# Optimization experiments

Hardware: AMD Instinct MI355X
Metric: run time of the kernel (lower is better)

The kernel has to match this reference:

```python
import jax, jax.numpy as jnp
import numpy as np
from jax import lax

N_QUBITS = 8
N_BLOCKS = 5

_H = jnp.array([[1.0, 1.0], [1.0, -1.0]], dtype=jnp.complex64) / np.sqrt(2.0).astype(np.float32)
# torchquantum PauliY.diagonalizing_gates = [Z, S, H] applied in order -> matrix H @ S @ Z = H @ diag(1, -1j)
_YROT = _H @ jnp.diag(jnp.array([1.0, -1j], dtype=jnp.complex64))


def apply_gate(st, U, wires):
    # st: [N, 2, 2, ..., 2] (n_qubits trailing axes); U: [2^k, 2^k]
    k = len(wires)
    axes = [w + 1 for w in wires]
    s = jnp.moveaxis(st, axes, list(range(1, k + 1)))
    shp = s.shape
    s = s.reshape(shp[0], 2 ** k, -1)
    s = jnp.einsum('ij,bjr->bir', U, s)
    return jnp.moveaxis(s.reshape(shp), list(range(1, k + 1)), axes)


def u3_mat(th, ph, lam):
    c = jnp.cos(0.5 * th).astype(jnp.complex64)
    s = jnp.sin(0.5 * th).astype(jnp.complex64)
    el = jnp.exp(1j * lam)
    ep = jnp.exp(1j * ph)
    return jnp.stack([jnp.stack([c, -el * s]), jnp.stack([ep * s, ep * el * c])])


def cu3_mat(th, ph, lam):
    M = jnp.eye(4, dtype=jnp.complex64)
    return M.at[2:, 2:].set(u3_mat(th, ph, lam))


def z_expvals(st):
    # <Z_w> for every wire from marginal probabilities
    n = st.ndim - 1
    mag = st.real ** 2 + st.imag ** 2
    outs = []
    for w in range(n):
        axes = tuple(a for a in range(1, n + 1) if a != w + 1)
        p = mag.sum(axes)  # [N, 2]
        outs.append(p[:, 0] - p[:, 1])
    return jnp.stack(outs, axis=1)


def quantum_conv(x, conv_w, conv_b, u3_params, cu3_params, fc_w, fc_b):
    n = N_QUBITS
    B, C, H, W = x.shape
    y = lax.conv_general_dilated(x, conv_w, (1, 1), 'SAME',
                                 dimension_numbers=('NCHW', 'OIHW', 'NCHW'))
    y = y + conv_b[None, :, None, None]
    ang = y.transpose(0, 2, 3, 1).reshape(-1, n)  # [B*H*W, n_qubits]
    Npx = ang.shape[0]
    # RY(theta)|0> encoding: product state of [cos(t/2), sin(t/2)] per wire
    c = jnp.cos(0.5 * ang)
    s = jnp.sin(0.5 * ang)
    st = jnp.stack([c[:, 0], s[:, 0]], axis=1).astype(jnp.complex64)
    for w in range(1, n):
        q = jnp.stack([c[:, w], s[:, w]], axis=1).astype(jnp.complex64)
        st = (st[:, :, None] * q[:, None, :]).reshape(Npx, -1)
    st = st.reshape((Npx,) + (2,) * n)
    # U3CU3Layer0: per block, U3 on each wire then circular CU3 ring
    for b in range(N_BLOCKS):
        for w in range(n):
            st = apply_gate(st, u3_mat(u3_params[b, w, 0], u3_params[b, w, 1], u3_params[b, w, 2]), [w])
        for w in range(n):
            st = apply_gate(st, cu3_mat(cu3_params[b, w, 0], cu3_params[b, w, 1], cu3_params[b, w, 2]), [w, (w + 1) % n])
    # MeasureAll(Z), then MeasureAll(X) and MeasureAll(Y) which MUTATE the device
    # state with their diagonalizing gates (torchquantum semantics)
    mz = z_expvals(st)
    for w in range(n):
        st = apply_gate(st, _H, [w])
    mx = z_expvals(st)
    for w in range(n):
        st = apply_gate(st, _YROT, [w])
    my = z_expvals(st)
    meas = jnp.concatenate([mz, mx, my], axis=1)  # [B*H*W, 3*n]
    out = meas @ fc_w.T + fc_b
    return out.reshape(B, H, W, -1).transpose(0, 3, 1, 2)


def setup_inputs() -> dict:
    key = jax.random.key(0)
    ks = jax.random.split(key, 7)
    n, cin, cout = N_QUBITS, 16, 32
    x = jax.random.normal(ks[0], (4, cin, 64, 64), dtype=jnp.float32)
    conv_w = jax.random.normal(ks[1], (n, cin, 3, 3), dtype=jnp.float32) / np.sqrt(cin * 9)
    conv_b = jax.random.normal(ks[2], (n,), dtype=jnp.float32) * 0.01
    u3_params = jax.random.uniform(ks[3], (N_BLOCKS, n, 3), dtype=jnp.float32, minval=-np.pi, maxval=np.pi)
    cu3_params = jax.random.uniform(ks[4], (N_BLOCKS, n, 3), dtype=jnp.float32, minval=-np.pi, maxval=np.pi)
    fc_w = jax.random.normal(ks[5], (cout, 3 * n), dtype=jnp.float32) / np.sqrt(3 * n)
    fc_b = jax.random.normal(ks[6], (cout,), dtype=jnp.float32) * 0.01
    return {'x': x, 'conv_w': conv_w, 'conv_b': conv_b, 'u3_params': u3_params,
            'cu3_params': cu3_params, 'fc_w': fc_w, 'fc_b': fc_b}


def reference(x, conv_w, conv_b, u3_params, cu3_params, fc_w, fc_b):
    return quantum_conv(x, conv_w, conv_b, u3_params, cu3_params, fc_w, fc_b)
```

## Files before the change

### kernel.cpp

```cpp
#include <hip/hip_runtime.h>

typedef float v2f __attribute__((ext_vector_type(2)));

template<int C>
__device__ __forceinline__ float dppmov(float x) {
  return __int_as_float(__builtin_amdgcn_update_dpp(0, __float_as_int(x), C, 0xF, 0xF, true));
}
template<int IMM>
__device__ __forceinline__ float dswz(float x) {
  return __int_as_float(__builtin_amdgcn_ds_swizzle(__float_as_int(x), IMM));
}
__device__ __forceinline__ float bperm(float x, int a) {
  return __int_as_float(__builtin_amdgcn_ds_bpermute(a, __float_as_int(x)));
}
template<int M>
__device__ __forceinline__ float bfly(float x) {
  if constexpr (M == 1)      return dppmov<0xB1>(x);
  else if constexpr (M == 2) return dppmov<0x4E>(x);
  else if constexpr (M == 8) return dppmov<0x128>(x);
  else                       return dswz<0x101F>(x);
}
template<int M>
__device__ __forceinline__ v2f bfly2(v2f v) {
  v2f o; o.x = bfly<M>(v.x); o.y = bfly<M>(v.y); return o;
}
__device__ __forceinline__ v2f sp(float s) { v2f v; v.x = s; v.y = s; return v; }
__device__ __forceinline__ v2f vfma(v2f a, v2f b, v2f c) {
  return __builtin_elementwise_fma(a, b, c);
}

template<int M, int CM>
__device__ __forceinline__ void crossG(v2f Sr[16], v2f Si[16],
    const float* g, int lane) {
  const bool hi = (lane & M) != 0;
  float fr, fi, gr, gi;
  if constexpr (CM == 0) {
    fr = hi ? g[6] : g[0]; fi = hi ? g[7] : g[1];
    gr = hi ? g[4] : g[2]; gi = hi ? g[5] : g[3];
  } else {
    const bool ct = (lane & CM) != 0;
    float f0r = hi ? g[6]  : g[0],  f0i = hi ? g[7]  : g[1];
    float g0r = hi ? g[4]  : g[2],  g0i = hi ? g[5]  : g[3];
    float f1r = hi ? g[14] : g[8],  f1i = hi ? g[15] : g[9];
    float g1r = hi ? g[12] : g[10], g1i = hi ? g[13] : g[11];
    fr = ct ? f1r : f0r; fi = ct ? f1i : f0i;
    gr = ct ? g1r : g0r; gi = ct ? g1i : g0i;
  }
  v2f vfr = sp(fr), vfi = sp(fi), vgr = sp(gr), vgi = sp(gi);
  v2f vfiN = sp(-fi), vgiN = sp(-gi);
#pragma unroll
  for (int r = 0; r < 16; ++r) {
    v2f pR = bfly2<M>(Sr[r]);
    v2f pI = bfly2<M>(Si[r]);
    v2f nR = vfma(vgiN, pI, vfma(vgr, pR, vfma(vfiN, Si[r], vfr * Sr[r])));
    v2f nI = vfma(vgi,  pR, vfma(vgr, pI, vfma(vfi,  Sr[r], vfr * Si[r])));
    Sr[r] = nR; Si[r] = nI;
  }
}

__device__ __forceinline__ void mixP(v2f& x0r, v2f& x0i, v2f& x1r, v2f& x1i,
    float m0r, float m0i, float m1r, float m1i,
    float m2r, float m2i, float m3r, float m3i) {
  v2f n0r = vfma(sp(-m1i), x1i, vfma(sp(m1r), x1r, vfma(sp(-m0i), x0i, sp(m0r) * x0r)));
  v2f n0i = vfma(sp( m1i), x1r, vfma(sp(m1r), x1i, vfma(sp( m0i), x0r, sp(m0r) * x0i)));
  v2f n1r = vfma(sp(-m3i), x1i, vfma(sp(m3r), x1r, vfma(sp(-m2i), x0i, sp(m2r) * x0r)));
  v2f n1i = vfma(sp( m3i), x1r, vfma(sp(m3r), x1i, vfma(sp( m2i), x0r, sp(m2r) * x0i)));
  x0r = n0r; x0i = n0i; x1r = n1r; x1i = n1i;
}

__device__ __forceinline__ void f4N(v2f Sr[16], v2f Si[16],
    const float* g, int lane) {
  const bool ct = (lane & 1) != 0;
  float m[8];
#pragma unroll
  for (int jj = 0; jj < 8; ++jj) m[jj] = ct ? g[8 + jj] : g[jj];
#pragma unroll
  for (int r = 0; r < 8; ++r)
    mixP(Sr[r], Si[r], Sr[r + 8], Si[r + 8],
         m[0], m[1], m[2], m[3], m[4], m[5], m[6], m[7]);
}
__device__ __forceinline__ void f5N(v2f Sr[16], v2f Si[16], const float* g) {
#pragma unroll
  for (int r = 0; r < 4; ++r)
    mixP(Sr[r], Si[r], Sr[r + 4], Si[r + 4],
         g[0], g[1], g[2], g[3], g[4], g[5], g[6], g[7]);
#pragma unroll
  for (int r = 8; r < 12; ++r)
    mixP(Sr[r], Si[r], Sr[r + 4], Si[r + 4],
         g[8], g[9], g[10], g[11], g[12], g[13], g[14], g[15]);
}
__device__ __forceinline__ void f6N(v2f Sr[16], v2f Si[16], const float* g) {
#pragma unroll
  for (int t = 0; t < 4; ++t) {
    const int r0 = (t >> 1) * 8 + (t & 1);
    mixP(Sr[r0], Si[r0], Sr[r0 + 2], Si[r0 + 2],
         g[0], g[1], g[2], g[3], g[4], g[5], g[6], g[7]);
    const int r1 = r0 + 4;
    mixP(Sr[r1], Si[r1], Sr[r1 + 2], Si[r1 + 2],
         g[8], g[9], g[10], g[11], g[12], g[13], g[14], g[15]);
  }
}
__device__ __forceinline__ void f7N(v2f Sr[16], v2f Si[16], const float* g) {
#pragma unroll
  for (int t = 0; t < 4; ++t) {
    const int r0 = t * 4;
    mixP(Sr[r0], Si[r0], Sr[r0 + 1], Si[r0 + 1],
         g[0], g[1], g[2], g[3], g[4], g[5], g[6], g[7]);
    const int r1 = r0 + 2;
    mixP(Sr[r1], Si[r1], Sr[r1 + 1], Si[r1 + 1],
         g[8], g[9], g[10], g[11], g[12], g[13], g[14], g[15]);
  }
}
__device__ __forceinline__ void f8pN(v2f Sr[16], v2f Si[16],
    const float* g, int lane) {
  const bool hi = (lane & 8) != 0;
  float fr[2], fi[2], gr[2], gi[2];
  fr[0] = hi ? g[6]  : g[0];  fi[0] = hi ? g[7]  : g[1];
  gr[0] = hi ? g[4]  : g[2];  gi[0] = hi ? g[5]  : g[3];
  fr[1] = hi ? g[14] : g[8];  fi[1] = hi ? g[15] : g[9];
  gr[1] = hi ? g[12] : g[10]; gi[1] = hi ? g[13] : g[11];
#pragma unroll
  for (int r = 0; r < 16; ++r) {
    const int m = r & 1;
    v2f pR = bfly2<8>(Sr[r]);
    v2f pI = bfly2<8>(Si[r]);
    v2f nR = vfma(sp(-gi[m]), pI, vfma(sp(gr[m]), pR, vfma(sp(-fi[m]), Si[r], sp(fr[m]) * Sr[r])));
    v2f nI = vfma(sp( gi[m]), pR, vfma(sp(gr[m]), pI, vfma(sp( fi[m]), Sr[r], sp(fr[m]) * Si[r])));
    Sr[r] = nR; Si[r] = nI;
  }
}
__device__ __forceinline__ void f8N(v2f Sr[16], v2f Si[16],
    const float* g, int lane) {
  const bool hi = (lane & 8) != 0;
  const float fr = hi ? g[6] : g[0], fi = hi ? g[7] : g[1];
  const float gr = hi ? g[4] : g[2], gi = hi ? g[5] : g[3];
#pragma unroll
  for (int r = 1; r < 16; r += 2) {
    v2f pR = bfly2<8>(Sr[r]);
    v2f pI = bfly2<8>(Si[r]);
    v2f nR = vfma(sp(-gi), pI, vfma(sp(gr), pR, vfma(sp(-fi), Si[r], sp(fr) * Sr[r])));
    v2f nI = vfma(sp( gi), pR, vfma(sp(gr), pI, vfma(sp( fi), Sr[r], sp(fr) * Si[r])));
    Sr[r] = nR; Si[r] = nI;
  }
}

template<int M>
__device__ __forceinline__ void crossO(const v2f Sr[16], const v2f Si[16],
                                       v2f& re, v2f& im) {
  v2f r = sp(0.0f), i = sp(0.0f);
#pragma unroll
  for (int k = 0; k < 16; ++k) {
    v2f pr = bfly2<M>(Sr[k]);
    v2f pi = bfly2<M>(Si[k]);
    r = vfma(Sr[k], pr, r);
    r = vfma(Si[k], pi, r);
    i = vfma(Si[k], pr, i);
    i = vfma(-Sr[k], pi, i);
  }
  re = r; im = i;
}

__device__ __forceinline__ void mm2(const float* A, const float* B, float* D) {
  D[0] = A[0]*B[0] - A[1]*B[1] + A[2]*B[4] - A[3]*B[5];
  D[1] = A[0]*B[1] + A[1]*B[0] + A[2]*B[5] + A[3]*B[4];
  D[2] = A[0]*B[2] - A[1]*B[3] + A[2]*B[6] - A[3]*B[7];
  D[3] = A[0]*B[3] + A[1]*B[2] + A[2]*B[7] + A[3]*B[6];
  D[4] = A[4]*B[0] - A[5]*B[1] + A[6]*B[4] - A[7]*B[5];
  D[5] = A[4]*B[1] + A[5]*B[0] + A[6]*B[5] + A[7]*B[4];
  D[6] = A[4]*B[2] - A[5]*B[3] + A[6]*B[6] - A[7]*B[7];
  D[7] = A[4]*B[3] + A[5]*B[2] + A[6]*B[7] + A[7]*B[6];
}
__device__ __forceinline__ void u3fill(const float* src, float* o) {
  float th = src[0], ph = src[1], lam = src[2];
  float c = cosf(0.5f * th), s = sinf(0.5f * th);
  float cl = cosf(lam), sl = sinf(lam);
  float cp = cosf(ph), spv = sinf(ph);
  float cpl = cosf(ph + lam), spl = sinf(ph + lam);
  o[0] = c;        o[1] = 0.0f;
  o[2] = -cl * s;  o[3] = -sl * s;
  o[4] = cp * s;   o[5] = spv * s;
  o[6] = cpl * c;  o[7] = spl * c;
}

__global__ __launch_bounds__(256) void qconv_kernel(
    const float* __restrict__ x, const float* __restrict__ cw,
    const float* __restrict__ cb, const float* __restrict__ u3p,
    const float* __restrict__ cu3p, const float* __restrict__ fcw,
    const float* __restrict__ fcb, float* __restrict__ out) {
  __shared__ float Us[40][8];
  __shared__ float Cs[40][8];
  __shared__ float Gs[640];
  __shared__ float FCWs[768];

  {
    const int t = threadIdx.x;
    if (t < 40) u3fill(u3p + t * 3, Us[t]);
    if (t >= 64 && t < 104) u3fill(cu3p + (t - 64) * 3, Cs[t - 64]);
    __syncthreads();
    if (t == 0) {
#pragma unroll
      for (int j = 0; j < 8; ++j) Gs[j] = Us[0][j];
    } else if (t < 36) {
      int j = t - 1, b = j / 7, k = j % 7;
      float* dst = Gs + 8 + b * 112 + k * 16;
      const float* U = Us[b * 8 + k + 1];
      const float* C = Cs[b * 8 + k];
#pragma unroll
      for (int u = 0; u < 8; ++u) dst[u] = U[u];
      mm2(C, U, dst + 8);
    } else if (t < 40) {
      int b = t - 36;
      float* dst = Gs + 568 + b * 16;
      const float* U = Us[(b + 1) * 8];
      const float* C = Cs[b * 8 + 7];
#pragma unroll
      for (int u = 0; u < 8; ++u) dst[u] = U[u];
      mm2(U, C, dst + 8);
    } else if (t == 40) {
#pragma unroll
      for (int j = 0; j < 8; ++j) Gs[632 + j] = Cs[39][j];
    }
    for (int i = t; i < 768; i += 256) {
      int tt = i % 24;
      int stage = tt >> 3, w = tt & 7;
      float sc = (stage >= 1 && w >= 4) ? 2.0f : 1.0f;
      FCWs[i] = fcw[i] * sc;
    }
    __syncthreads();
  }

  const int lane = threadIdx.x & 63;
  const int wid = __builtin_amdgcn_readfirstlane(
      (int)((blockIdx.x * blockDim.x + threadIdx.x) >> 6));
  const int p0 = wid * 8;
  const int q = lane & 15;

  float ang;
  {
    const int px = lane >> 3;
    const int oc = lane & 7;
    const int p  = p0 + px;
    const int b  = p >> 12;
    const int hh = (p >> 6) & 63;
    const int wim = p & 63;
    float acc = cb[oc];
#pragma unroll 4
    for (int ic = 0; ic < 16; ++ic) {
      const float* wp = cw + (oc * 16 + ic) * 9;
      const float* xp = x + (b * 16 + ic) * 4096;
#pragma unroll
      for (int kh = 0; kh < 3; ++kh) {
        int ih = hh + kh - 1;
        bool rok = (unsigned)ih < 64u;
        int ihc = rok ? ih : 0;
#pragma unroll
        for (int kw = 0; kw < 3; ++kw) {
          int iw = wim + kw - 1;
          bool ok = rok && ((unsigned)iw < 64u);
          int iwc = ((unsigned)iw < 64u) ? iw : 0;
          float xv = xp[ihc * 64 + iwc];
          acc = fmaf(ok ? xv : 0.0f, wp[kh * 3 + kw], acc);
        }
      }
    }
    ang = acc;
  }

  v2f Sr[16], Si[16];
  {
    const int gb = (lane & 48) << 2;
    float aA[8], aB[8];
#pragma unroll
    for (int w = 0; w < 8; ++w) {
      aA[w] = bperm(ang, gb + (w << 2));
      aB[w] = bperm(ang, gb + ((8 + w) << 2));
    }
    float cA[8], sA[8], cB[8], sB[8];
#pragma unroll
    for (int w = 0; w < 8; ++w) {
      __sincosf(0.5f * aA[w], &sA[w], &cA[w]);
      __sincosf(0.5f * aB[w], &sB[w], &cB[w]);
    }
    v2f c0; c0.x = cA[0]; c0.y = cB[0];
    v2f s0; s0.x = sA[0]; s0.y = sB[0];
    v2f c0r = vfma(sp(Gs[2]), s0, sp(Gs[0]) * c0);
    v2f c0i = vfma(sp(Gs[3]), s0, sp(Gs[1]) * c0);
    v2f s0r = vfma(sp(Gs[6]), s0, sp(Gs[4]) * c0);
    v2f s0i = vfma(sp(Gs[7]), s0, sp(Gs[5]) * c0);
    const bool w0 = (q & 8) != 0;
    v2f selR = w0 ? s0r : c0r;
    v2f selI = w0 ? s0i : c0i;
    float fA = ((q & 4) ? sA[1] : cA[1]) * ((q & 2) ? sA[2] : cA[2])
             * ((q & 1) ? sA[3] : cA[3]);
    float fB = ((q & 4) ? sB[1] : cB[1]) * ((q & 2) ? sB[2] : cB[2])
             * ((q & 1) ? sB[3] : cB[3]);
    v2f uu[4], vv[4];
    uu[0].x = cA[6]*cA[7]; uu[1].x = cA[6]*sA[7];
    uu[2].x = sA[6]*cA[7]; uu[3].x = sA[6]*sA[7];
    uu[0].y = cB[6]*cB[7]; uu[1].y = cB[6]*sB[7];
    uu[2].y = sB[6]*cB[7]; uu[3].y = sB[6]*sB[7];
    float vA0 = fA * cA[4], vA1 = fA * sA[4];
    float vB0 = fB * cB[4], vB1 = fB * sB[4];
    vv[0].x = vA0*cA[5]; vv[1].x = vA0*sA[5];
    vv[2].x = vA1*cA[5]; vv[3].x = vA1*sA[5];
    vv[0].y = vB0*cB[5]; vv[1].y = vB0*sB[5];
    vv[2].y = vB1*cB[5]; vv[3].y = vB1*sB[5];
#pragma unroll
    for (int r = 0; r < 16; ++r) {
      v2f base = vv[r >> 2] * uu[r & 3];
      Sr[r] = selR * base;
      Si[r] = selI * base;
    }
  }

  for (int b = 0; b < 5; ++b) {
    const float* base = Gs + 8 + b * 112;
    crossG<4, 8>(Sr, Si, base +  0, lane);
    crossG<2, 4>(Sr, Si, base + 16, lane);
    crossG<1, 2>(Sr, Si, base + 32, lane);
    f4N(Sr, Si, base + 48, lane);
    f5N(Sr, Si, base + 64);
    f6N(Sr, Si, base + 80);
    f7N(Sr, Si, base + 96);
    if (b < 4) f8pN(Sr, Si, Gs + 568 + b * 16, lane);
  }
  f8N(Sr, Si, Gs + 632, lane);

  float sg[4];
  sg[0] = (q & 8) ? -1.0f : 1.0f;
  sg[1] = (q & 4) ? -1.0f : 1.0f;
  sg[2] = (q & 2) ? -1.0f : 1.0f;
  sg[3] = (q & 1) ? -1.0f : 1.0f;

  v2f PT[24];
  {
    v2f re0, im0, re1, im1, re2, im2, re3, im3;
    crossO<8>(Sr, Si, re0, im0);
    crossO<4>(Sr, Si, re1, im1);
    crossO<2>(Sr, Si, re2, im2);
    crossO<1>(Sr, Si, re3, im3);
    PT[8]  = re0; PT[9]  = re1; PT[10] = re2; PT[11] = re3;
    PT[16] = sp(sg[0]) * im0; PT[17] = sp(sg[1]) * im1;
    PT[18] = sp(sg[2]) * im2; PT[19] = sp(sg[3]) * im3;

    v2f P[16];
#pragma unroll
    for (int r = 0; r < 16; ++r) P[r] = vfma(Si[r], Si[r], Sr[r] * Sr[r]);
    v2f t01[8];
#pragma unroll
    for (int k = 0; k < 8; ++k) t01[k] = P[2*k] + P[2*k+1];
    v2f q0 = t01[0] + t01[1], q1 = t01[2] + t01[3];
    v2f q2 = t01[4] + t01[5], q3 = t01[6] + t01[7];
    v2f h0 = q0 + q1, h1 = q2 + q3;
    v2f p  = h0 + h1;
    PT[4] = h0 - h1;
    PT[5] = (q0 - q1) + (q2 - q3);
    PT[6] = (t01[0]-t01[1]) + (t01[2]-t01[3])
          + (t01[4]-t01[5]) + (t01[6]-t01[7]);
    PT[7] = (P[0]-P[1]) + (P[2]-P[3]) + (P[4]-P[5]) + (P[6]-P[7])
          + (P[8]-P[9]) + (P[10]-P[11]) + (P[12]-P[13]) + (P[14]-P[15]);
    PT[0] = sp(sg[0]) * p; PT[1] = sp(sg[1]) * p;
    PT[2] = sp(sg[2]) * p; PT[3] = sp(sg[3]) * p;

    v2f re, im;
    re = sp(0.0f); im = sp(0.0f);
#pragma unroll
    for (int r = 0; r < 8; ++r) {
      re = vfma(Sr[r], Sr[r+8], re); re = vfma(Si[r], Si[r+8], re);
      im = vfma(Si[r], Sr[r+8], im); im = vfma(-Sr[r], Si[r+8], im);
    }
    PT[12] = re; PT[20] = im;
    re = sp(0.0f); im = sp(0.0f);
#pragma unroll
    for (int t = 0; t < 8; ++t) {
      const int lo = (t & 3) + (t >> 2) * 8;
      re = vfma(Sr[lo], Sr[lo+4], re); re = vfma(Si[lo], Si[lo+4], re);
      im = vfma(Si[lo], Sr[lo+4], im); im = vfma(-Sr[lo], Si[lo+4], im);
    }
    PT[13] = re; PT[21] = im;
    re = sp(0.0f); im = sp(0.0f);
#pragma unroll
    for (int t = 0; t < 8; ++t) {
      const int lo = (t & 1) + (t >> 1) * 4;
      re = vfma(Sr[lo], Sr[lo+2], re); re = vfma(Si[lo], Si[lo+2], re);
      im = vfma(Si[lo], Sr[lo+2], im); im = vfma(-Sr[lo], Si[lo+2], im);
    }
    PT[14] = re; PT[22] = im;
    re = sp(0.0f); im = sp(0.0f);
#pragma unroll
    for (int t = 0; t < 8; ++t) {
      const int lo = 2 * t;
      re = vfma(Sr[lo], Sr[lo+1], re); re = vfma(Si[lo], Si[lo+1], re);
      im = vfma(Si[lo], Sr[lo+1], im); im = vfma(-Sr[lo], Si[lo+1], im);
    }
    PT[15] = re; PT[23] = im;
  }

  const int j = q & 7;
  const bool isB = (q & 8) != 0;
  float mm[24];
#pragma unroll
  for (int t = 0; t < 24; ++t) {
    v2f v = PT[t] + bfly2<8>(PT[t]);
    float s = isB ? v.y : v.x;
    s += bfly<1>(s);
    s += bfly<2>(s);
    s += bfly<4>(s);
    mm[t] = s;
  }

  const int g = lane >> 4;
  const int p = p0 + 2 * g + (isB ? 1 : 0);
  const int ob = (p >> 12) * 131072 + (p & 4095);
#pragma unroll
  for (int k = 0; k < 4; ++k) {
    const int ch = 4 * j + k;
    const float* wr = FCWs + ch * 24;
    float acc = fcb[ch];
#pragma unroll
    for (int u = 0; u < 24; ++u) acc = fmaf(mm[u], wr[u], acc);
    out[ob + ch * 4096] = acc;
  }
}

extern "C" void kernel_launch(void* const* d_in, const int* in_sizes, int n_in,
                              void* d_out, int out_size, void* d_ws, size_t ws_size,
                              hipStream_t stream) {
  const float* x      = (const float*)d_in[0];
  const float* conv_w = (const float*)d_in[1];
  const float* conv_b = (const float*)d_in[2];
  const float* u3p    = (const float*)d_in[3];
  const float* cu3p   = (const float*)d_in[4];
  const float* fcw    = (const float*)d_in[5];
  const float* fcb    = (const float*)d_in[6];
  float* out = (float*)d_out;

  qconv_kernel<<<512, 256, 0, stream>>>(x, conv_w, conv_b, u3p, cu3p,
                                        fcw, fcb, out);
}
```

Before: 107.0 us.

## Fuse adjacent two-qubit gate stages into precomputed 4x4 combined matrices

```diff
diff --git a/kernel.cpp b/kernel.cpp
--- a/kernel.cpp
+++ b/kernel.cpp
@@ -17,6 +17,7 @@
 __device__ __forceinline__ float bfly(float x) {
   if constexpr (M == 1)      return dppmov<0xB1>(x);
   else if constexpr (M == 2) return dppmov<0x4E>(x);
+  else if constexpr (M == 3) return dppmov<0x1B>(x);
   else if constexpr (M == 8) return dppmov<0x128>(x);
   else                       return dswz<0x101F>(x);
 }
@@ -68,6 +69,31 @@
   x0r = n0r; x0i = n0i; x1r = n1r; x1i = n1i;
 }
 
+__device__ __forceinline__ void f23N(v2f Sr[16], v2f Si[16],
+    const float* tab, int lane) {
+  const int idx = ((lane >> 2) & 1) * 4 + (lane & 3);
+  const float* rp = tab + idx * 8;
+  const float c0r = rp[0], c0i = rp[1], c1r = rp[2], c1i = rp[3];
+  const float c2r = rp[4], c2i = rp[5], c3r = rp[6], c3i = rp[7];
+#pragma unroll
+  for (int r = 0; r < 16; ++r) {
+    v2f p1R = bfly2<1>(Sr[r]), p1I = bfly2<1>(Si[r]);
+    v2f p2R = bfly2<2>(Sr[r]), p2I = bfly2<2>(Si[r]);
+    v2f p3R = bfly2<3>(Sr[r]), p3I = bfly2<3>(Si[r]);
+    v2f nR = sp(c0r) * Sr[r];
+    nR = vfma(sp(-c0i), Si[r], nR);
+    nR = vfma(sp( c1r), p1R, nR);  nR = vfma(sp(-c1i), p1I, nR);
+    nR = vfma(sp( c2r), p2R, nR);  nR = vfma(sp(-c2i), p2I, nR);
+    nR = vfma(sp( c3r), p3R, nR);  nR = vfma(sp(-c3i), p3I, nR);
+    v2f nI = sp(c0i) * Sr[r];
+    nI = vfma(sp(c0r), Si[r], nI);
+    nI = vfma(sp(c1i), p1R, nI);   nI = vfma(sp(c1r), p1I, nI);
+    nI = vfma(sp(c2i), p2R, nI);   nI = vfma(sp(c2r), p2I, nI);
+    nI = vfma(sp(c3i), p3R, nI);   nI = vfma(sp(c3r), p3I, nI);
+    Sr[r] = nR; Si[r] = nI;
+  }
+}
+
 __device__ __forceinline__ void f4N(v2f Sr[16], v2f Si[16],
     const float* g, int lane) {
   const bool ct = (lane & 1) != 0;
@@ -89,26 +115,34 @@
     mixP(Sr[r], Si[r], Sr[r + 4], Si[r + 4],
          g[8], g[9], g[10], g[11], g[12], g[13], g[14], g[15]);
 }
-__device__ __forceinline__ void f6N(v2f Sr[16], v2f Si[16], const float* g) {
-#pragma unroll
-  for (int t = 0; t < 4; ++t) {
-    const int r0 = (t >> 1) * 8 + (t & 1);
-    mixP(Sr[r0], Si[r0], Sr[r0 + 2], Si[r0 + 2],
-         g[0], g[1], g[2], g[3], g[4], g[5], g[6], g[7]);
-    const int r1 = r0 + 4;
-    mixP(Sr[r1], Si[r1], Sr[r1 + 2], Si[r1 + 2],
-         g[8], g[9], g[10], g[11], g[12], g[13], g[14], g[15]);
-  }
-}
-__device__ __forceinline__ void f7N(v2f Sr[16], v2f Si[16], const float* g) {
-#pragma unroll
-  for (int t = 0; t < 4; ++t) {
-    const int r0 = t * 4;
-    mixP(Sr[r0], Si[r0], Sr[r0 + 1], Si[r0 + 1],
-         g[0], g[1], g[2], g[3], g[4], g[5], g[6], g[7]);
-    const int r1 = r0 + 2;
-    mixP(Sr[r1], Si[r1], Sr[r1 + 1], Si[r1 + 1],
-         g[8], g[9], g[10], g[11], g[12], g[13], g[14], g[15]);
+__device__ __forceinline__ void f67N(v2f Sr[16], v2f Si[16], const float* T) {
+#pragma unroll
+  for (int qd = 0; qd < 4; ++qd) {
+    const int B = qd * 4;
+    const float* M = T + (qd & 1) * 32;
+    v2f ar0 = Sr[B+0], ai0 = Si[B+0], ar1 = Sr[B+1], ai1 = Si[B+1];
+    v2f ar2 = Sr[B+2], ai2 = Si[B+2], ar3 = Sr[B+3], ai3 = Si[B+3];
+#pragma unroll
+    for (int rp = 0; rp < 4; ++rp) {
+      const float* Mr = M + rp * 8;
+      v2f nR = sp(Mr[0]) * ar0;
+      nR = vfma(sp(-Mr[1]), ai0, nR);
+      nR = vfma(sp( Mr[2]), ar1, nR);
+      nR = vfma(sp(-Mr[3]), ai1, nR);
+      nR = vfma(sp( Mr[4]), ar2, nR);
+      nR = vfma(sp(-Mr[5]), ai2, nR);
+      nR = vfma(sp( Mr[6]), ar3, nR);
+      nR = vfma(sp(-Mr[7]), ai3, nR);
+      v2f nI = sp(Mr[1]) * ar0;
+      nI = vfma(sp(Mr[0]), ai0, nI);
+      nI = vfma(sp(Mr[3]), ar1, nI);
+      nI = vfma(sp(Mr[2]), ai1, nI);
+      nI = vfma(sp(Mr[5]), ar2, nI);
+      nI = vfma(sp(Mr[4]), ai2, nI);
+      nI = vfma(sp(Mr[7]), ar3, nI);
+      nI = vfma(sp(Mr[6]), ai3, nI);
+      Sr[B + rp] = nR; Si[B + rp] = nI;
+    }
   }
 }
 __device__ __forceinline__ void f8pN(v2f Sr[16], v2f Si[16],
@@ -191,11 +225,19 @@
   __shared__ float Cs[40][8];
   __shared__ float Gs[640];
   __shared__ float FCWs[768];
+  __shared__ float F23t[320];
+  __shared__ float F67t[320];
 
   {
     const int t = threadIdx.x;
     if (t < 40) u3fill(u3p + t * 3, Us[t]);
     if (t >= 64 && t < 104) u3fill(cu3p + (t - 64) * 3, Cs[t - 64]);
+    for (int i = t; i < 768; i += 256) {
+      int tt = i % 24;
+      int stage = tt >> 3, w = tt & 7;
+      float sc = (stage >= 1 && w >= 4) ? 2.0f : 1.0f;
+      FCWs[i] = fcw[i] * sc;
+    }
     __syncthreads();
     if (t == 0) {
 #pragma unroll
@@ -220,11 +262,38 @@
 #pragma unroll
       for (int j = 0; j < 8; ++j) Gs[632 + j] = Cs[39][j];
     }
-    for (int i = t; i < 768; i += 256) {
-      int tt = i % 24;
-      int stage = tt >> 3, w = tt & 7;
-      float sc = (stage >= 1 && w >= 4) ? 2.0f : 1.0f;
-      FCWs[i] = fcw[i] * sc;
+    __syncthreads();
+    if (t < 40) {
+      int b = t >> 3, idx = t & 7;
+      int ct = idx >> 2, row = idx & 3;
+      const float* M2 = Gs + 8 + b * 112 + 16 + ct * 8;
+      int w2p = row >> 1, w3p = row & 1;
+      const float* M3 = Gs + 8 + b * 112 + 32 + w2p * 8;
+      float* dst = F23t + b * 64 + idx * 8;
+#pragma unroll
+      for (int k = 0; k < 4; ++k) {
+        int w2 = w2p ^ (k >> 1), w3 = w3p ^ (k & 1);
+        float a_r = M2[(w2p * 2 + w2) * 2], a_i = M2[(w2p * 2 + w2) * 2 + 1];
+        float b_r = M3[(w3p * 2 + w3) * 2], b_i = M3[(w3p * 2 + w3) * 2 + 1];
+        dst[k * 2]     = a_r * b_r - a_i * b_i;
+        dst[k * 2 + 1] = a_r * b_i + a_i * b_r;
+      }
+    } else if (t >= 64 && t < 104) {
+      int u = t - 64;
+      int b = u >> 3, idx = u & 7;
+      int ct = idx >> 2, rp = idx & 3;
+      const float* M6 = Gs + 8 + b * 112 + 80 + ct * 8;
+      int b1p = rp >> 1, b0p = rp & 1;
+      const float* M7 = Gs + 8 + b * 112 + 96 + b1p * 8;
+      float* dst = F67t + b * 64 + ct * 32 + rp * 8;
+#pragma unroll
+      for (int c = 0; c < 4; ++c) {
+        int b1 = c >> 1, b0 = c & 1;
+        float a_r = M6[(b1p * 2 + b1) * 2], a_i = M6[(b1p * 2 + b1) * 2 + 1];
+        float b_r = M7[(b0p * 2 + b0) * 2], b_i = M7[(b0p * 2 + b0) * 2 + 1];
+        dst[c * 2]     = a_r * b_r - a_i * b_i;
+        dst[c * 2 + 1] = a_r * b_i + a_i * b_r;
+      }
     }
     __syncthreads();
   }
@@ -315,13 +384,11 @@
 
   for (int b = 0; b < 5; ++b) {
     const float* base = Gs + 8 + b * 112;
-    crossG<4, 8>(Sr, Si, base +  0, lane);
-    crossG<2, 4>(Sr, Si, base + 16, lane);
-    crossG<1, 2>(Sr, Si, base + 32, lane);
+    crossG<4, 8>(Sr, Si, base + 0, lane);
+    f23N(Sr, Si, F23t + b * 64, lane);
     f4N(Sr, Si, base + 48, lane);
     f5N(Sr, Si, base + 64);
-    f6N(Sr, Si, base + 80);
-    f7N(Sr, Si, base + 96);
+    f67N(Sr, Si, F67t + b * 64);
     if (b < 4) f8pN(Sr, Si, Gs + 568 + b * 16, lane);
   }
   f8N(Sr, Si, Gs + 632, lane);
```

New measurement: 106.5 us. No clear change (-0.4%).

## Process two independent pixel groups per wavefront to raise ILP

Applied to the files above, without the earlier changes.

```diff
diff --git a/kernel.cpp b/kernel.cpp
--- a/kernel.cpp
+++ b/kernel.cpp
@@ -30,8 +30,8 @@
 }
 
 template<int M, int CM>
-__device__ __forceinline__ void crossG(v2f Sr[16], v2f Si[16],
-    const float* g, int lane) {
+__device__ __forceinline__ void crossGD(v2f Pr[16], v2f Pi[16],
+    v2f Qr[16], v2f Qi[16], const float* g, int lane) {
   const bool hi = (lane & M) != 0;
   float fr, fi, gr, gi;
   if constexpr (CM == 0) {
@@ -50,11 +50,15 @@
   v2f vfiN = sp(-fi), vgiN = sp(-gi);
 #pragma unroll
   for (int r = 0; r < 16; ++r) {
-    v2f pR = bfly2<M>(Sr[r]);
-    v2f pI = bfly2<M>(Si[r]);
-    v2f nR = vfma(vgiN, pI, vfma(vgr, pR, vfma(vfiN, Si[r], vfr * Sr[r])));
-    v2f nI = vfma(vgi,  pR, vfma(vgr, pI, vfma(vfi,  Sr[r], vfr * Si[r])));
-    Sr[r] = nR; Si[r] = nI;
+    v2f pR = bfly2<M>(Pr[r]);
+    v2f pI = bfly2<M>(Pi[r]);
+    v2f qR = bfly2<M>(Qr[r]);
+    v2f qI = bfly2<M>(Qi[r]);
+    v2f nPR = vfma(vgiN, pI, vfma(vgr, pR, vfma(vfiN, Pi[r], vfr * Pr[r])));
+    v2f nPI = vfma(vgi,  pR, vfma(vgr, pI, vfma(vfi,  Pr[r], vfr * Pi[r])));
+    v2f nQR = vfma(vgiN, qI, vfma(vgr, qR, vfma(vfiN, Qi[r], vfr * Qr[r])));
+    v2f nQI = vfma(vgi,  qR, vfma(vgr, qI, vfma(vfi,  Qr[r], vfr * Qi[r])));
+    Pr[r] = nPR; Pi[r] = nPI; Qr[r] = nQR; Qi[r] = nQI;
   }
 }
 
@@ -68,51 +72,71 @@
   x0r = n0r; x0i = n0i; x1r = n1r; x1i = n1i;
 }
 
-__device__ __forceinline__ void f4N(v2f Sr[16], v2f Si[16],
-    const float* g, int lane) {
+__device__ __forceinline__ void f4D(v2f Pr[16], v2f Pi[16],
+    v2f Qr[16], v2f Qi[16], const float* g, int lane) {
   const bool ct = (lane & 1) != 0;
   float m[8];
 #pragma unroll
   for (int jj = 0; jj < 8; ++jj) m[jj] = ct ? g[8 + jj] : g[jj];
 #pragma unroll
-  for (int r = 0; r < 8; ++r)
-    mixP(Sr[r], Si[r], Sr[r + 8], Si[r + 8],
+  for (int r = 0; r < 8; ++r) {
+    mixP(Pr[r], Pi[r], Pr[r + 8], Pi[r + 8],
          m[0], m[1], m[2], m[3], m[4], m[5], m[6], m[7]);
-}
-__device__ __forceinline__ void f5N(v2f Sr[16], v2f Si[16], const float* g) {
-#pragma unroll
-  for (int r = 0; r < 4; ++r)
-    mixP(Sr[r], Si[r], Sr[r + 4], Si[r + 4],
+    mixP(Qr[r], Qi[r], Qr[r + 8], Qi[r + 8],
+         m[0], m[1], m[2], m[3], m[4], m[5], m[6], m[7]);
+  }
+}
+__device__ __forceinline__ void f5D(v2f Pr[16], v2f Pi[16],
+    v2f Qr[16], v2f Qi[16], const float* g) {
+#pragma unroll
+  for (int r = 0; r < 4; ++r) {
+    mixP(Pr[r], Pi[r], Pr[r + 4], Pi[r + 4],
          g[0], g[1], g[2], g[3], g[4], g[5], g[6], g[7]);
-#pragma unroll
-  for (int r = 8; r < 12; ++r)
-    mixP(Sr[r], Si[r], Sr[r + 4], Si[r + 4],
+    mixP(Qr[r], Qi[r], Qr[r + 4], Qi[r + 4],
+         g[0], g[1], g[2], g[3], g[4], g[5], g[6], g[7]);
+  }
+#pragma unroll
+  for (int r = 8; r < 12; ++r) {
+    mixP(Pr[r], Pi[r], Pr[r + 4], Pi[r + 4],
          g[8], g[9], g[10], g[11], g[12], g[13], g[14], g[15]);
-}
-__device__ __forceinline__ void f6N(v2f Sr[16], v2f Si[16], const float* g) {
+    mixP(Qr[r], Qi[r], Qr[r + 4], Qi[r + 4],
+         g[8], g[9], g[10], g[11], g[12], g[13], g[14], g[15]);
+  }
+}
+__device__ __forceinline__ void f6D(v2f Pr[16], v2f Pi[16],
+    v2f Qr[16], v2f Qi[16], const float* g) {
 #pragma unroll
   for (int t = 0; t < 4; ++t) {
     const int r0 = (t >> 1) * 8 + (t & 1);
-    mixP(Sr[r0], Si[r0], Sr[r0 + 2], Si[r0 + 2],
+    mixP(Pr[r0], Pi[r0], Pr[r0 + 2], Pi[r0 + 2],
+         g[0], g[1], g[2], g[3], g[4], g[5], g[6], g[7]);
+    mixP(Qr[r0], Qi[r0], Qr[r0 + 2], Qi[r0 + 2],
          g[0], g[1], g[2], g[3], g[4], g[5], g[6], g[7]);
     const int r1 = r0 + 4;
-    mixP(Sr[r1], Si[r1], Sr[r1 + 2], Si[r1 + 2],
+    mixP(Pr[r1], Pi[r1], Pr[r1 + 2], Pi[r1 + 2],
          g[8], g[9], g[10], g[11], g[12], g[13], g[14], g[15]);
-  }
-}
-__device__ __forceinline__ void f7N(v2f Sr[16], v2f Si[16], const float* g) {
+    mixP(Qr[r1], Qi[r1], Qr[r1 + 2], Qi[r1 + 2],
+         g[8], g[9], g[10], g[11], g[12], g[13], g[14], g[15]);
+  }
+}
+__device__ __forceinline__ void f7D(v2f Pr[16], v2f Pi[16],
+    v2f Qr[16], v2f Qi[16], const float* g) {
 #pragma unroll
   for (int t = 0; t < 4; ++t) {
     const int r0 = t * 4;
-    mixP(Sr[r0], Si[r0], Sr[r0 + 1], Si[r0 + 1],
+    mixP(Pr[r0], Pi[r0], Pr[r0 + 1], Pi[r0 + 1],
+         g[0], g[1], g[2], g[3], g[4], g[5], g[6], g[7]);
+    mixP(Qr[r0], Qi[r0], Qr[r0 + 1], Qi[r0 + 1],
          g[0], g[1], g[2], g[3], g[4], g[5], g[6], g[7]);
     const int r1 = r0 + 2;
-    mixP(Sr[r1], Si[r1], Sr[r1 + 1], Si[r1 + 1],
+    mixP(Pr[r1], Pi[r1], Pr[r1 + 1], Pi[r1 + 1],
          g[8], g[9], g[10], g[11], g[12], g[13], g[14], g[15]);
-  }
-}
-__device__ __forceinline__ void f8pN(v2f Sr[16], v2f Si[16],
-    const float* g, int lane) {
+    mixP(Qr[r1], Qi[r1], Qr[r1 + 1], Qi[r1 + 1],
+         g[8], g[9], g[10], g[11], g[12], g[13], g[14], g[15]);
+  }
+}
+__device__ __forceinline__ void f8pD(v2f Pr[16], v2f Pi[16],
+    v2f Qr[16], v2f Qi[16], const float* g, int lane) {
   const bool hi = (lane & 8) != 0;
   float fr[2], fi[2], gr[2], gi[2];
   fr[0] = hi ? g[6]  : g[0];  fi[0] = hi ? g[7]  : g[1];
@@ -122,25 +146,33 @@
 #pragma unroll
   for (int r = 0; r < 16; ++r) {
     const int m = r & 1;
-    v2f pR = bfly2<8>(Sr[r]);
-    v2f pI = bfly2<8>(Si[r]);
-    v2f nR = vfma(sp(-gi[m]), pI, vfma(sp(gr[m]), pR, vfma(sp(-fi[m]), Si[r], sp(fr[m]) * Sr[r])));
-    v2f nI = vfma(sp( gi[m]), pR, vfma(sp(gr[m]), pI, vfma(sp( fi[m]), Sr[r], sp(fr[m]) * Si[r])));
-    Sr[r] = nR; Si[r] = nI;
-  }
-}
-__device__ __forceinline__ void f8N(v2f Sr[16], v2f Si[16],
-    const float* g, int lane) {
+    v2f pR = bfly2<8>(Pr[r]);
+    v2f pI = bfly2<8>(Pi[r]);
+    v2f qR = bfly2<8>(Qr[r]);
+    v2f qI = bfly2<8>(Qi[r]);
+    v2f nPR = vfma(sp(-gi[m]), pI, vfma(sp(gr[m]), pR, vfma(sp(-fi[m]), Pi[r], sp(fr[m]) * Pr[r])));
+    v2f nPI = vfma(sp( gi[m]), pR, vfma(sp(gr[m]), pI, vfma(sp( fi[m]), Pr[r], sp(fr[m]) * Pi[r])));
+    v2f nQR = vfma(sp(-gi[m]), qI, vfma(sp(gr[m]), qR, vfma(sp(-fi[m]), Qi[r], sp(fr[m]) * Qr[r])));
+    v2f nQI = vfma(sp( gi[m]), qR, vfma(sp(gr[m]), qI, vfma(sp( fi[m]), Qr[r], sp(fr[m]) * Qi[r])));
+    Pr[r] = nPR; Pi[r] = nPI; Qr[r] = nQR; Qi[r] = nQI;
+  }
+}
+__device__ __forceinline__ void f8D(v2f Pr[16], v2f Pi[16],
+    v2f Qr[16], v2f Qi[16], const float* g, int lane) {
   const bool hi = (lane & 8) != 0;
   const float fr = hi ? g[6] : g[0], fi = hi ? g[7] : g[1];
   const float gr = hi ? g[4] : g[2], gi = hi ? g[5] : g[3];
 #pragma unroll
   for (int r = 1; r < 16; r += 2) {
-    v2f pR = bfly2<8>(Sr[r]);
-    v2f pI = bfly2<8>(Si[r]);
-    v2f nR = vfma(sp(-gi), pI, vfma(sp(gr), pR, vfma(sp(-fi), Si[r], sp(fr) * Sr[r])));
-    v2f nI = vfma(sp( gi), pR, vfma(sp(gr), pI, vfma(sp( fi), Sr[r], sp(fr) * Si[r])));
-    Sr[r] = nR; Si[r] = nI;
+    v2f pR = bfly2<8>(Pr[r]);
+    v2f pI = bfly2<8>(Pi[r]);
+    v2f qR = bfly2<8>(Qr[r]);
+    v2f qI = bfly2<8>(Qi[r]);
+    v2f nPR = vfma(sp(-gi), pI, vfma(sp(gr), pR, vfma(sp(-fi), Pi[r], sp(fr) * Pr[r])));
+    v2f nPI = vfma(sp( gi), pR, vfma(sp(gr), pI, vfma(sp( fi), Pr[r], sp(fr) * Pi[r])));
+    v2f nQR = vfma(sp(-gi), qI, vfma(sp(gr), qR, vfma(sp(-fi), Qi[r], sp(fr) * Qr[r])));
+    v2f nQI = vfma(sp( gi), qR, vfma(sp(gr), qI, vfma(sp( fi), Qr[r], sp(fr) * Qi[r])));
+    Pr[r] = nPR; Pi[r] = nPI; Qr[r] = nQR; Qi[r] = nQI;
   }
 }
 
@@ -158,6 +190,109 @@
     i = vfma(-Sr[k], pi, i);
   }
   re = r; im = i;
+}
+
+__device__ __forceinline__ void partials(const v2f Sr[16], const v2f Si[16],
+                                         const float* sg, v2f PT[24]) {
+  v2f re0, im0, re1, im1, re2, im2, re3, im3;
+  crossO<8>(Sr, Si, re0, im0);
+  crossO<4>(Sr, Si, re1, im1);
+  crossO<2>(Sr, Si, re2, im2);
+  crossO<1>(Sr, Si, re3, im3);
+  PT[8]  = re0; PT[9]  = re1; PT[10] = re2; PT[11] = re3;
+  PT[16] = sp(sg[0]) * im0; PT[17] = sp(sg[1]) * im1;
+  PT[18] = sp(sg[2]) * im2; PT[19] = sp(sg[3]) * im3;
+
+  v2f P[16];
+#pragma unroll
+  for (int r = 0; r < 16; ++r) P[r] = vfma(Si[r], Si[r], Sr[r] * Sr[r]);
+  v2f t01[8];
+#pragma unroll
+  for (int k = 0; k < 8; ++k) t01[k] = P[2*k] + P[2*k+1];
+  v2f q0 = t01[0] + t01[1], q1 = t01[2] + t01[3];
+  v2f q2 = t01[4] + t01[5], q3 = t01[6] + t01[7];
+  v2f h0 = q0 + q1, h1 = q2 + q3;
+  v2f p  = h0 + h1;
+  PT[4] = h0 - h1;
+  PT[5] = (q0 - q1) + (q2 - q3);
+  PT[6] = (t01[0]-t01[1]) + (t01[2]-t01[3]) + (t01[4]-t01[5]) + (t01[6]-t01[7]);
+  PT[7] = (P[0]-P[1]) + (P[2]-P[3]) + (P[4]-P[5]) + (P[6]-P[7])
+        + (P[8]-P[9]) + (P[10]-P[11]) + (P[12]-P[13]) + (P[14]-P[15]);
+  PT[0] = sp(sg[0]) * p; PT[1] = sp(sg[1]) * p;
+  PT[2] = sp(sg[2]) * p; PT[3] = sp(sg[3]) * p;
+
+  v2f re, im;
+  re = sp(0.0f); im = sp(0.0f);
+#pragma unroll
+  for (int r = 0; r < 8; ++r) {
+    re = vfma(Sr[r], Sr[r+8], re); re = vfma(Si[r], Si[r+8], re);
+    im = vfma(Si[r], Sr[r+8], im); im = vfma(-Sr[r], Si[r+8], im);
+  }
+  PT[12] = re; PT[20] = im;
+  re = sp(0.0f); im = sp(0.0f);
+#pragma unroll
+  for (int t = 0; t < 8; ++t) {
+    const int lo = (t & 3) + (t >> 2) * 8;
+    re = vfma(Sr[lo], Sr[lo+4], re); re = vfma(Si[lo], Si[lo+4], re);
+    im = vfma(Si[lo], Sr[lo+4], im); im = vfma(-Sr[lo], Si[lo+4], im);
+  }
+  PT[13] = re; PT[21] = im;
+  re = sp(0.0f); im = sp(0.0f);
+#pragma unroll
+  for (int t = 0; t < 8; ++t) {
+    const int lo = (t & 1) + (t >> 1) * 4;
+    re = vfma(Sr[lo], Sr[lo+2], re); re = vfma(Si[lo], Si[lo+2], re);
+    im = vfma(Si[lo], Sr[lo+2], im); im = vfma(-Sr[lo], Si[lo+2], im);
+  }
+  PT[14] = re; PT[22] = im;
+  re = sp(0.0f); im = sp(0.0f);
+#pragma unroll
+  for (int t = 0; t < 8; ++t) {
+    const int lo = 2 * t;
+    re = vfma(Sr[lo], Sr[lo+1], re); re = vfma(Si[lo], Si[lo+1], re);
+    im = vfma(Si[lo], Sr[lo+1], im); im = vfma(-Sr[lo], Si[lo+1], im);
+  }
+  PT[15] = re; PT[23] = im;
+}
+
+__device__ __forceinline__ void initChain(const float aA[8], const float aB[8],
+    const float* Gs, int q, v2f Sr[16], v2f Si[16]) {
+  float cA[8], sA[8], cB[8], sB[8];
+#pragma unroll
+  for (int w = 0; w < 8; ++w) {
+    __sincosf(0.5f * aA[w], &sA[w], &cA[w]);
+    __sincosf(0.5f * aB[w], &sB[w], &cB[w]);
+  }
+  v2f c0; c0.x = cA[0]; c0.y = cB[0];
+  v2f s0; s0.x = sA[0]; s0.y = sB[0];
+  v2f c0r = vfma(sp(Gs[2]), s0, sp(Gs[0]) * c0);
+  v2f c0i = vfma(sp(Gs[3]), s0, sp(Gs[1]) * c0);
+  v2f s0r = vfma(sp(Gs[6]), s0, sp(Gs[4]) * c0);
+  v2f s0i = vfma(sp(Gs[7]), s0, sp(Gs[5]) * c0);
+  const bool w0 = (q & 8) != 0;
+  v2f selR = w0 ? s0r : c0r;
+  v2f selI = w0 ? s0i : c0i;
+  float fA = ((q & 4) ? sA[1] : cA[1]) * ((q & 2) ? sA[2] : cA[2])
+           * ((q & 1) ? sA[3] : cA[3]);
+  float fB = ((q & 4) ? sB[1] : cB[1]) * ((q & 2) ? sB[2] : cB[2])
+           * ((q & 1) ? sB[3] : cB[3]);
+  v2f uu[4], vv[4];
+  uu[0].x = cA[6]*cA[7]; uu[1].x = cA[6]*sA[7];
+  uu[2].x = sA[6]*cA[7]; uu[3].x = sA[6]*sA[7];
+  uu[0].y = cB[6]*cB[7]; uu[1].y = cB[6]*sB[7];
+  uu[2].y = sB[6]*cB[7]; uu[3].y = sB[6]*sB[7];
+  float vA0 = fA * cA[4], vA1 = fA * sA[4];
+  float vB0 = fB * cB[4], vB1 = fB * sB[4];
+  vv[0].x = vA0*cA[5]; vv[1].x = vA0*sA[5];
+  vv[2].x = vA1*cA[5]; vv[3].x = vA1*sA[5];
+  vv[0].y = vB0*cB[5]; vv[1].y = vB0*sB[5];
+  vv[2].y = vB1*cB[5]; vv[3].y = vB1*sB[5];
+#pragma unroll
+  for (int r = 0; r < 16; ++r) {
+    v2f base = vv[r >> 2] * uu[r & 3];
+    Sr[r] = selR * base;
+    Si[r] = selI * base;
+  }
 }
 
 __device__ __forceinline__ void mm2(const float* A, const float* B, float* D) {
@@ -196,6 +331,12 @@
     const int t = threadIdx.x;
     if (t < 40) u3fill(u3p + t * 3, Us[t]);
     if (t >= 64 && t < 104) u3fill(cu3p + (t - 64) * 3, Cs[t - 64]);
+    for (int i = t; i < 768; i += 256) {
+      int tt = i % 24;
+      int stage = tt >> 3, w = tt & 7;
+      float sc = (stage >= 1 && w >= 4) ? 2.0f : 1.0f;
+      FCWs[i] = fcw[i] * sc;
+    }
     __syncthreads();
     if (t == 0) {
 #pragma unroll
@@ -220,30 +361,24 @@
 #pragma unroll
       for (int j = 0; j < 8; ++j) Gs[632 + j] = Cs[39][j];
     }
-    for (int i = t; i < 768; i += 256) {
-      int tt = i % 24;
-      int stage = tt >> 3, w = tt & 7;
-      float sc = (stage >= 1 && w >= 4) ? 2.0f : 1.0f;
-      FCWs[i] = fcw[i] * sc;
-    }
     __syncthreads();
   }
 
   const int lane = threadIdx.x & 63;
   const int wid = __builtin_amdgcn_readfirstlane(
       (int)((blockIdx.x * blockDim.x + threadIdx.x) >> 6));
-  const int p0 = wid * 8;
+  const int p0 = wid * 16;
   const int q = lane & 15;
 
-  float ang;
+  float ang1, ang2;
   {
     const int px = lane >> 3;
     const int oc = lane & 7;
     const int p  = p0 + px;
     const int b  = p >> 12;
     const int hh = (p >> 6) & 63;
-    const int wim = p & 63;
-    float acc = cb[oc];
+    const int w1 = p & 63;
+    float acc1 = cb[oc], acc2 = acc1;
 #pragma unroll 4
     for (int ic = 0; ic < 16; ++ic) {
       const float* wp = cw + (oc * 16 + ic) * 9;
@@ -253,78 +388,54 @@
         int ih = hh + kh - 1;
         bool rok = (unsigned)ih < 64u;
         int ihc = rok ? ih : 0;
+        const float* row = xp + ihc * 64;
 #pragma unroll
         for (int kw = 0; kw < 3; ++kw) {
-          int iw = wim + kw - 1;
-          bool ok = rok && ((unsigned)iw < 64u);
-          int iwc = ((unsigned)iw < 64u) ? iw : 0;
-          float xv = xp[ihc * 64 + iwc];
-          acc = fmaf(ok ? xv : 0.0f, wp[kh * 3 + kw], acc);
+          float wv = wp[kh * 3 + kw];
+          int iw1 = w1 + kw - 1;
+          int iw2 = iw1 + 8;
+          bool ok1 = rok && ((unsigned)iw1 < 64u);
+          bool ok2 = rok && ((unsigned)iw2 < 64u);
+          float x1 = row[(unsigned)iw1 < 64u ? iw1 : 0];
+          float x2 = row[(unsigned)iw2 < 64u ? iw2 : 0];
+          acc1 = fmaf(ok1 ? x1 : 0.0f, wv, acc1);
+          acc2 = fmaf(ok2 ? x2 : 0.0f, wv, acc2);
         }
       }
     }
-    ang = acc;
-  }
-
-  v2f Sr[16], Si[16];
+    ang1 = acc1; ang2 = acc2;
+  }
+
+  v2f Pr[16], Pi[16], Qr[16], Qi[16];
   {
     const int gb = (lane & 48) << 2;
     float aA[8], aB[8];
 #pragma unroll
     for (int w = 0; w < 8; ++w) {
-      aA[w] = bperm(ang, gb + (w << 2));
-      aB[w] = bperm(ang, gb + ((8 + w) << 2));
+      aA[w] = bperm(ang1, gb + (w << 2));
+      aB[w] = bperm(ang1, gb + ((8 + w) << 2));
     }
-    float cA[8], sA[8], cB[8], sB[8];
+    initChain(aA, aB, Gs, q, Pr, Pi);
 #pragma unroll
     for (int w = 0; w < 8; ++w) {
-      __sincosf(0.5f * aA[w], &sA[w], &cA[w]);
-      __sincosf(0.5f * aB[w], &sB[w], &cB[w]);
+      aA[w] = bperm(ang2, gb + (w << 2));
+      aB[w] = bperm(ang2, gb + ((8 + w) << 2));
     }
-    v2f c0; c0.x = cA[0]; c0.y = cB[0];
-    v2f s0; s0.x = sA[0]; s0.y = sB[0];
-    v2f c0r = vfma(sp(Gs[2]), s0, sp(Gs[0]) * c0);
-    v2f c0i = vfma(sp(Gs[3]), s0, sp(Gs[1]) * c0);
-    v2f s0r = vfma(sp(Gs[6]), s0, sp(Gs[4]) * c0);
-    v2f s0i = vfma(sp(Gs[7]), s0, sp(Gs[5]) * c0);
-    const bool w0 = (q & 8) != 0;
-    v2f selR = w0 ? s0r : c0r;
-    v2f selI = w0 ? s0i : c0i;
-    float fA = ((q & 4) ? sA[1] : cA[1]) * ((q & 2) ? sA[2] : cA[2])
-             * ((q & 1) ? sA[3] : cA[3]);
-    float fB = ((q & 4) ? sB[1] : cB[1]) * ((q & 2) ? sB[2] : cB[2])
-             * ((q & 1) ? sB[3] : cB[3]);
-    v2f uu[4], vv[4];
-    uu[0].x = cA[6]*cA[7]; uu[1].x = cA[6]*sA[7];
-    uu[2].x = sA[6]*cA[7]; uu[3].x = sA[6]*sA[7];
-    uu[0].y = cB[6]*cB[7]; uu[1].y = cB[6]*sB[7];
-    uu[2].y = sB[6]*cB[7]; uu[3].y = sB[6]*sB[7];
-    float vA0 = fA * cA[4], vA1 = fA * sA[4];
-    float vB0 = fB * cB[4], vB1 = fB * sB[4];
-    vv[0].x = vA0*cA[5]; vv[1].x = vA0*sA[5];
-    vv[2].x = vA1*cA[5]; vv[3].x = vA1*sA[5];
-    vv[0].y = vB0*cB[5]; vv[1].y = vB0*sB[5];
-    vv[2].y = vB1*cB[5]; vv[3].y = vB1*sB[5];
-#pragma unroll
-    for (int r = 0; r < 16; ++r) {
-      v2f base = vv[r >> 2] * uu[r & 3];
-      Sr[r] = selR * base;
-      Si[r] = selI * base;
-    }
+    initChain(aA, aB, Gs, q, Qr, Qi);
   }
 
   for (int b = 0; b < 5; ++b) {
     const float* base = Gs + 8 + b * 112;
-    crossG<4, 8>(Sr, Si, base +  0, lane);
-    crossG<2, 4>(Sr, Si, base + 16, lane);
-    crossG<1, 2>(Sr, Si, base + 32, lane);
-    f4N(Sr, Si, base + 48, lane);
-    f5N(Sr, Si, base + 64);
-    f6N(Sr, Si, base + 80);
-    f7N(Sr, Si, base + 96);
-    if (b < 4) f8pN(Sr, Si, Gs + 568 + b * 16, lane);
-  }
-  f8N(Sr, Si, Gs + 632, lane);
+    crossGD<4, 8>(Pr, Pi, Qr, Qi, base +  0, lane);
+    crossGD<2, 4>(Pr, Pi, Qr, Qi, base + 16, lane);
+    crossGD<1, 2>(Pr, Pi, Qr, Qi, base + 32, lane);
+    f4D(Pr, Pi, Qr, Qi, base + 48, lane);
+    f5D(Pr, Pi, Qr, Qi, base + 64);
+    f6D(Pr, Pi, Qr, Qi, base + 80);
+    f7D(Pr, Pi, Qr, Qi, base + 96);
+    if (b < 4) f8pD(Pr, Pi, Qr, Qi, Gs + 568 + b * 16, lane);
+  }
+  f8D(Pr, Pi, Qr, Qi, Gs + 632, lane);
 
   float sg[4];
   sg[0] = (q & 8) ? -1.0f : 1.0f;
@@ -332,94 +443,44 @@
   sg[2] = (q & 2) ? -1.0f : 1.0f;
   sg[3] = (q & 1) ? -1.0f : 1.0f;
 
-  v2f PT[24];
-  {
-    v2f re0, im0, re1, im1, re2, im2, re3, im3;
-    crossO<8>(Sr, Si, re0, im0);
-    crossO<4>(Sr, Si, re1, im1);
-    crossO<2>(Sr, Si, re2, im2);
-    crossO<1>(Sr, Si, re3, im3);
-    PT[8]  = re0; PT[9]  = re1; PT[10] = re2; PT[11] = re3;
-    PT[16] = sp(sg[0]) * im0; PT[17] = sp(sg[1]) * im1;
-    PT[18] = sp(sg[2]) * im2; PT[19] = sp(sg[3]) * im3;
-
-    v2f P[16];
-#pragma unroll
-    for (int r = 0; r < 16; ++r) P[r] = vfma(Si[r], Si[r], Sr[r] * Sr[r]);
-    v2f t01[8];
-#pragma unroll
-    for (int k = 0; k < 8; ++k) t01[k] = P[2*k] + P[2*k+1];
-    v2f q0 = t01[0] + t01[1], q1 = t01[2] + t01[3];
-    v2f q2 = t01[4] + t01[5], q3 = t01[6] + t01[7];
-    v2f h0 = q0 + q1, h1 = q2 + q3;
-    v2f p  = h0 + h1;
-    PT[4] = h0 - h1;
-    PT[5] = (q0 - q1) + (q2 - q3);
-    PT[6] = (t01[0]-t01[1]) + (t01[2]-t01[3])
-          + (t01[4]-t01[5]) + (t01[6]-t01[7]);
-    PT[7] = (P[0]-P[1]) + (P[2]-P[3]) + (P[4]-P[5]) + (P[6]-P[7])
-          + (P[8]-P[9]) + (P[10]-P[11]) + (P[12]-P[13]) + (P[14]-P[15]);
-    PT[0] = sp(sg[0]) * p; PT[1] = sp(sg[1]) * p;
-    PT[2] = sp(sg[2]) * p; PT[3] = sp(sg[3]) * p;
-
-    v2f re, im;
-    re = sp(0.0f); im = sp(0.0f);
-#pragma unroll
-    for (int r = 0; r < 8; ++r) {
-      re = vfma(Sr[r], Sr[r+8], re); re = vfma(Si[r], Si[r+8], re);
-      im = vfma(Si[r], Sr[r+8], im); im = vfma(-Sr[r], Si[r+8], im);
-    }
-    PT[12] = re; PT[20] = im;
-    re = sp(0.0f); im = sp(0.0f);
-#pragma unroll
-    for (int t = 0; t < 8; ++t) {
-      const int lo = (t & 3) + (t >> 2) * 8;
-      re = vfma(Sr[lo], Sr[lo+4], re); re = vfma(Si[lo], Si[lo+4], re);
-      im = vfma(Si[lo], Sr[lo+4], im); im = vfma(-Sr[lo], Si[lo+4], im);
-    }
-    PT[13] = re; PT[21] = im;
-    re = sp(0.0f); im = sp(0.0f);
-#pragma unroll
-    for (int t = 0; t < 8; ++t) {
-      const int lo = (t & 1) + (t >> 1) * 4;
-      re = vfma(Sr[lo], Sr[lo+2], re); re = vfma(Si[lo], Si[lo+2], re);
-      im = vfma(Si[lo], Sr[lo+2], im); im = vfma(-Sr[lo], Si[lo+2], im);
-    }
-    PT[14] = re; PT[22] = im;
-    re = sp(0.0f); im = sp(0.0f);
-#pragma unroll
-    for (int t = 0; t < 8; ++t) {
-      const int lo = 2 * t;
-      re = vfma(Sr[lo], Sr[lo+1], re); re = vfma(Si[lo], Si[lo+1], re);
-      im = vfma(Si[lo], Sr[lo+1], im); im = vfma(-Sr[lo], Si[lo+1], im);
-    }
-    PT[15] = re; PT[23] = im;
-  }
-
   const int j = q & 7;
   const bool isB = (q & 8) != 0;
-  float mm[24];
+  const int g = lane >> 4;
+
+  v2f PT1[24], PT2[24];
+  partials(Pr, Pi, sg, PT1);
+  partials(Qr, Qi, sg, PT2);
+
+  float mm1[24], mm2v[24];
 #pragma unroll
   for (int t = 0; t < 24; ++t) {
-    v2f v = PT[t] + bfly2<8>(PT[t]);
-    float s = isB ? v.y : v.x;
-    s += bfly<1>(s);
-    s += bfly<2>(s);
-    s += bfly<4>(s);
-    mm[t] = s;
-  }
-
-  const int g = lane >> 4;
-  const int p = p0 + 2 * g + (isB ? 1 : 0);
-  const int ob = (p >> 12) * 131072 + (p & 4095);
+    v2f v1 = PT1[t] + bfly2<8>(PT1[t]);
+    v2f v2 = PT2[t] + bfly2<8>(PT2[t]);
+    float s1 = isB ? v1.y : v1.x;
+    float s2 = isB ? v2.y : v2.x;
+    s1 += bfly<1>(s1);  s2 += bfly<1>(s2);
+    s1 += bfly<2>(s1);  s2 += bfly<2>(s2);
+    s1 += bfly<4>(s1);  s2 += bfly<4>(s2);
+    mm1[t] = s1; mm2v[t] = s2;
+  }
+
+  const int pP = p0 + 2 * g + (isB ? 1 : 0);
+  const int pQ = pP + 8;
+  const int obP = (pP >> 12) * 131072 + (pP & 4095);
+  const int obQ = (pQ >> 12) * 131072 + (pQ & 4095);
 #pragma unroll
   for (int k = 0; k < 4; ++k) {
     const int ch = 4 * j + k;
     const float* wr = FCWs + ch * 24;
-    float acc = fcb[ch];
-#pragma unroll
-    for (int u = 0; u < 24; ++u) acc = fmaf(mm[u], wr[u], acc);
-    out[ob + ch * 4096] = acc;
+    float a1 = fcb[ch], a2 = a1;
+#pragma unroll
+    for (int u = 0; u < 24; ++u) {
+      float wv = wr[u];
+      a1 = fmaf(mm1[u], wv, a1);
+      a2 = fmaf(mm2v[u], wv, a2);
+    }
+    out[obP + ch * 4096] = a1;
+    out[obQ + ch * 4096] = a2;
   }
 }
 
@@ -435,6 +496,6 @@
   const float* fcb    = (const float*)d_in[6];
   float* out = (float*)d_out;
 
-  qconv_kernel<<<512, 256, 0, stream>>>(x, conv_w, conv_b, u3p, cu3p,
+  qconv_kernel<<<256, 256, 0, stream>>>(x, conv_w, conv_b, u3p, cu3p,
                                         fcw, fcb, out);
 }
```

New measurement: 110.2 us. +3.0%, slower.
